# Kernel optimization log

Measured on AMD Instinct MI355X. Metric: run time of the kernel, lower is better.

Reference implementation:

```python
import jax, jax.numpy as jnp
import numpy as np

DIM = 2048
N_HEADS = 16
N_KV = 8
NUM_REP = N_HEADS // N_KV  # 2
HEAD_DIM = DIM // N_HEADS // 2  # 64
EPS = 1e-5
THETA = 10000.0
B, S = 2, 2048


def setup_inputs() -> dict:
    key = jax.random.key(0)
    ks = jax.random.split(key, 12)
    x = jax.random.normal(ks[0], (B, S, DIM), dtype=jnp.float32)
    wq = jax.random.normal(ks[1], (DIM, DIM), dtype=jnp.float32) * 0.02
    wk = jax.random.normal(ks[2], (DIM, DIM // NUM_REP), dtype=jnp.float32) * 0.02
    wv = jax.random.normal(ks[3], (DIM, DIM // NUM_REP), dtype=jnp.float32) * 0.02
    wo = jax.random.normal(ks[4], (DIM, DIM), dtype=jnp.float32) * 0.02
    lambda_q1 = jax.random.normal(ks[5], (HEAD_DIM,), dtype=jnp.float32) * 0.1
    lambda_k1 = jax.random.normal(ks[6], (HEAD_DIM,), dtype=jnp.float32) * 0.1
    lambda_q2 = jax.random.normal(ks[7], (HEAD_DIM,), dtype=jnp.float32) * 0.1
    lambda_k2 = jax.random.normal(ks[8], (HEAD_DIM,), dtype=jnp.float32) * 0.1
    lambda_init = jnp.array([0.8], dtype=jnp.float32)
    subln_w = jnp.ones((2 * HEAD_DIM,), dtype=jnp.float32)
    # rope tables: precompute_freqs_cis(dim=2*HEAD_DIM) then sliced to first HEAD_DIM//2 freqs
    exps = jnp.arange(0, HEAD_DIM, 2, dtype=jnp.float32) / (2.0 * HEAD_DIM)
    freqs = THETA ** (-exps)  # [HEAD_DIM//2]
    ang = jnp.arange(S, dtype=jnp.float32)[:, None] * freqs[None, :]  # [S, HEAD_DIM//2]
    return {
        "x": x, "wq": wq, "wk": wk, "wv": wv, "wo": wo,
        "lambda_q1": lambda_q1, "lambda_k1": lambda_k1,
        "lambda_q2": lambda_q2, "lambda_k2": lambda_k2,
        "lambda_init": lambda_init, "subln_w": subln_w,
        "freqs_cos": jnp.cos(ang), "freqs_sin": jnp.sin(ang),
    }


def _rope(t, cos, sin):
    # t: [B,S,H,hd]; cos/sin: [S, hd//2]; complex-pair rotation on (even, odd)
    e, o = t[..., 0::2], t[..., 1::2]
    c = cos[None, :, None, :]
    s = sin[None, :, None, :]
    return jnp.stack([e * c - o * s, e * s + o * c], axis=-1).reshape(t.shape)


def _repeat_kv_buggy(t, n_rep):
    # faithful to source: t is [B, n_kv, S, hd]; unsqueeze at dim 3 then reshape,
    # which flattens (n_kv, S, rep) -> (n_kv*rep, S)
    b, n_kv, slen, hd = t.shape
    exp = jnp.broadcast_to(t[:, :, :, None, :], (b, n_kv, slen, n_rep, hd))
    return exp.reshape(b, n_kv * n_rep, slen, hd)


def _attn(q, k, v, scale):
    # q,k: [B,H,S,hd]; v: [B,H,S,2hd]
    scores = jnp.einsum('bhqd,bhkd->bhqk', q, k) * scale
    p = jax.nn.softmax(scores, axis=-1)
    return jnp.einsum('bhqk,bhkd->bhqd', p, v)


def reference(x, wq, wk, wv, wo, lambda_q1, lambda_k1, lambda_q2, lambda_k2,
              lambda_init, subln_w, freqs_cos, freqs_sin):
    bsz, seqlen, _ = x.shape
    scale = HEAD_DIM ** -0.5
    q = (x @ wq).reshape(bsz, seqlen, 2 * N_HEADS, HEAD_DIM)
    k = (x @ wk).reshape(bsz, seqlen, 2 * N_KV, HEAD_DIM)
    v = (x @ wv).reshape(bsz, seqlen, N_KV, 2 * HEAD_DIM)
    q = _rope(q, freqs_cos, freqs_sin)
    k = _rope(k, freqs_cos, freqs_sin)
    q = q.reshape(bsz, seqlen, N_HEADS, 2, HEAD_DIM)
    k = k.reshape(bsz, seqlen, N_KV, 2, HEAD_DIM)
    q1 = q[:, :, :, 0].transpose(0, 2, 1, 3)  # [B,H,S,hd]
    q2 = q[:, :, :, 1].transpose(0, 2, 1, 3)
    k1 = _repeat_kv_buggy(k[:, :, :, 0].transpose(0, 2, 1, 3), NUM_REP)
    k2 = _repeat_kv_buggy(k[:, :, :, 1].transpose(0, 2, 1, 3), NUM_REP)
    vr = _repeat_kv_buggy(v.transpose(0, 2, 1, 3), NUM_REP)  # [B,H,S,2hd]
    attn1 = _attn(q1, k1, vr, scale)
    attn2 = _attn(q2, k2, vr, scale)
    lambda_1 = jnp.exp(jnp.sum(lambda_q1 * lambda_k1))
    lambda_2 = jnp.exp(jnp.sum(lambda_q2 * lambda_k2))
    lambda_full = lambda_1 - lambda_2 + lambda_init[0]
    attn = attn1 - lambda_full * attn2  # [B,H,S,2hd]
    # sub-layer RMSNorm over 2*HEAD_DIM
    rms = jax.lax.rsqrt(jnp.mean(attn * attn, axis=-1, keepdims=True) + EPS)
    attn = attn * rms * subln_w
    attn = attn * (1.0 - lambda_init[0])
    attn = attn.transpose(0, 2, 1, 3).reshape(bsz, seqlen, N_HEADS * 2 * HEAD_DIM)
    return attn @ wo
```

## Files before the change

kernel.cpp:

```cpp
#include <hip/hip_runtime.h>
#include <stdint.h>

typedef unsigned short u16;
typedef __attribute__((ext_vector_type(8))) short bf16x8v;
typedef __attribute__((ext_vector_type(4))) float f32x4;

#define DIM   2048
#define NH    16
#define NKV   8
#define HD    64
#define B_    2
#define S_    2048
#define ROWS  (B_*S_)
#define NQKV  4096
#define EPS_   1e-5f
#define SCALE_ 0.125f

__device__ __forceinline__ u16 bfbits(float f) {
  union { float f; unsigned int u; } a; a.f = f;
  unsigned int u = a.u;
  return (u16)((u + 0x7FFFu + ((u >> 16) & 1u)) >> 16);
}

__device__ __forceinline__ f32x4 mfma16(bf16x8v a, bf16x8v b, f32x4 c) {
  return __builtin_amdgcn_mfma_f32_16x16x32_bf16(a, b, c, 0, 0, 0);
}

__device__ __forceinline__ void gload_lds16(const void* g, void* l) {
  __builtin_amdgcn_global_load_lds(
      (const __attribute__((address_space(1))) unsigned int*)g,
      (__attribute__((address_space(3))) unsigned int*)l, 16, 0, 0);
}

__global__ void cast_f32_bf16(const float* __restrict__ src, u16* __restrict__ dst, int n4) {
  int i = blockIdx.x * 256 + threadIdx.x;
  if (i >= n4) return;
  float4 v = ((const float4*)src)[i];
  ushort4 o; o.x = bfbits(v.x); o.y = bfbits(v.y); o.z = bfbits(v.z); o.w = bfbits(v.w);
  ((ushort4*)dst)[i] = o;
}

__global__ void transpose_cast(const float* __restrict__ src, u16* __restrict__ dst, int R, int C) {
  __shared__ float t[32][33];
  int c0 = blockIdx.x * 32, r0 = blockIdx.y * 32;
  int x = threadIdx.x, y = threadIdx.y;
#pragma unroll
  for (int i = 0; i < 4; ++i) t[y + 8*i][x] = src[(size_t)(r0 + y + 8*i) * C + c0 + x];
  __syncthreads();
#pragma unroll
  for (int i = 0; i < 4; ++i) dst[(size_t)(c0 + y + 8*i) * R + r0 + x] = bfbits(t[x][y + 8*i]);
}

__global__ void v_transpose(const float* __restrict__ qkv, u16* __restrict__ Vt) {
  __shared__ float t[32][33];
  int z = blockIdx.z;
  int b = z >> 3, kv = z & 7;
  int s0 = blockIdx.x * 32, d0 = blockIdx.y * 32;
  int x = threadIdx.x, y = threadIdx.y;
  const float* src = qkv + (size_t)b * S_ * NQKV + 3072 + kv * 128;
#pragma unroll
  for (int i = 0; i < 4; ++i) t[y + 8*i][x] = src[(size_t)(s0 + y + 8*i) * NQKV + d0 + x];
  __syncthreads();
  u16* dst = Vt + ((size_t)(b * NKV + kv) * 128) * S_;
#pragma unroll
  for (int i = 0; i < 4; ++i) dst[(size_t)(d0 + y + 8*i) * S_ + s0 + x] = bfbits(t[x][y + 8*i]);
}

__global__ void rope_kernel(const float* __restrict__ qkv, const float* __restrict__ fc,
                            const float* __restrict__ fs, u16* __restrict__ D1, u16* __restrict__ D2,
                            int hshift, int coloff) {
  int p = blockIdx.x * 256 + threadIdx.x;
  int i = p & 31;
  int hh = (p >> 5) & ((1 << hshift) - 1);
  int row = p >> (5 + hshift);
  int s = row & (S_ - 1);
  int b = row >> 11;
  const float* src = qkv + (size_t)row * NQKV + coloff + hh * HD + 2 * i;
  float e = src[0], o = src[1];
  float c = fc[s * 32 + i], sn = fs[s * 32 + i];
  float r0 = e * c - o * sn, r1 = e * sn + o * c;
  u16* dst = (hh & 1) ? D2 : D1;
  int nh = 1 << (hshift - 1);
  size_t offo = (((size_t)b * nh + (hh >> 1)) * S_ + s) * HD + 2 * i;
  unsigned int packed = (unsigned int)bfbits(r0) | ((unsigned int)bfbits(r1) << 16);
  *(unsigned int*)(dst + offo) = packed;
}

__global__ void lambda_kernel(const float* lq1, const float* lk1, const float* lq2,
                              const float* lk2, const float* li, float* scal) {
  int t = threadIdx.x;
  float p1 = lq1[t] * lk1[t];
  float p2 = lq2[t] * lk2[t];
#pragma unroll
  for (int off = 32; off > 0; off >>= 1) { p1 += __shfl_xor(p1, off); p2 += __shfl_xor(p2, off); }
  if (t == 0) {
    scal[0] = __expf(p1) - __expf(p2) + li[0];
    scal[1] = 1.0f - li[0];
  }
}

template<int NI>
__global__ __launch_bounds__(512, 2) void gemm8p(const u16* __restrict__ A, const u16* __restrict__ Bt,
                                                 float* __restrict__ C, int M, int N, int K) {
  constexpr int BN = NI * 64;
  constexpr int BROUNDS = BN / 64;
  __shared__ u16 Al[2][256 * 64];
  __shared__ u16 Bl[2][BN * 64];
  const int tid = threadIdx.x;
  const int wid = tid >> 6, lane = tid & 63;
  const int wm = wid >> 2, wn = wid & 3;
  const int lr = lane & 15, cq = lane >> 4;
  const size_t row0 = (size_t)blockIdx.y * 256, col0 = (size_t)blockIdx.x * BN;

  f32x4 acc[8][NI];
#pragma unroll
  for (int i = 0; i < 8; ++i)
#pragma unroll
    for (int j = 0; j < NI; ++j) acc[i][j] = f32x4{0.f, 0.f, 0.f, 0.f};

  bf16x8v a[4][2], b0[NI / 2][2], b1[NI / 2][2];

  auto stageA = [&](int buf, int kt) {
#pragma unroll
    for (int rd = 0; rd < 4; ++rd) {
      int n = rd * 512 + tid;
      int r = n >> 3, c = (n & 7) ^ (r & 7);
      gload_lds16(A + (row0 + r) * (size_t)K + kt + c * 8,
                  (char*)&Al[buf][0] + (rd * 512 + wid * 64) * 16);
    }
  };
  auto stageB = [&](int buf, int kt) {
#pragma unroll
    for (int rd = 0; rd < BROUNDS; ++rd) {
      int n = rd * 512 + tid;
      int r = n >> 3, c = (n & 7) ^ (r & 7);
      gload_lds16(Bt + (col0 + r) * (size_t)K + kt + c * 8,
                  (char*)&Bl[buf][0] + (rd * 512 + wid * 64) * 16);
    }
  };
  auto readA = [&](int buf, int mh) {
#pragma unroll
    for (int m2 = 0; m2 < 4; ++m2)
#pragma unroll
      for (int ks = 0; ks < 2; ++ks) {
        int rt = wm * 128 + (mh * 4 + m2) * 16 + lr;
        a[m2][ks] = *(const bf16x8v*)&Al[buf][rt * 64 + (((ks * 4 + cq) ^ (rt & 7)) * 8)];
      }
  };
  auto readB = [&](int buf, int nh, bf16x8v (&bb)[NI / 2][2]) {
#pragma unroll
    for (int n2 = 0; n2 < NI / 2; ++n2)
#pragma unroll
      for (int ks = 0; ks < 2; ++ks) {
        int rt = wn * (NI * 16) + (nh * (NI / 2) + n2) * 16 + lr;
        bb[n2][ks] = *(const bf16x8v*)&Bl[buf][rt * 64 + (((ks * 4 + cq) ^ (rt & 7)) * 8)];
      }
  };
  auto mfmaq = [&](int mh, int nh, bf16x8v (&bb)[NI / 2][2]) {
    __builtin_amdgcn_s_barrier();
    asm volatile("s_waitcnt lgkmcnt(0)" ::: "memory");
    __builtin_amdgcn_sched_barrier(0);
    __builtin_amdgcn_s_setprio(1);
#pragma unroll
    for (int m2 = 0; m2 < 4; ++m2)
#pragma unroll
      for (int n2 = 0; n2 < NI / 2; ++n2)
#pragma unroll
        for (int ks = 0; ks < 2; ++ks)
          acc[mh * 4 + m2][nh * (NI / 2) + n2] =
              mfma16(a[m2][ks], bb[n2][ks], acc[mh * 4 + m2][nh * (NI / 2) + n2]);
    __builtin_amdgcn_s_setprio(0);
    __builtin_amdgcn_s_barrier();
  };
  auto vmwait = [&](bool last) {
    if (last) { asm volatile("s_waitcnt vmcnt(0)" ::: "memory"); }
    else {
      if constexpr (NI == 4) { asm volatile("s_waitcnt vmcnt(4)" ::: "memory"); }
      else                   { asm volatile("s_waitcnt vmcnt(2)" ::: "memory"); }
    }
  };

  stageA(0, 0);
  stageB(0, 0);
  stageB(1, 64);
  vmwait(false);
  __builtin_amdgcn_s_barrier();

  const int NITER = K >> 7;
  for (int it = 0; it < NITER; ++it) {
    const int kt = it << 7;
    const bool nl = (it < NITER - 1);
    readA(0, 0); readB(0, 0, b0);
    mfmaq(0, 0, b0);
    readB(0, 1, b1);
    stageA(1, kt + 64);
    mfmaq(0, 1, b1);
    readA(0, 1);
    if (nl) stageB(0, kt + 128);
    mfmaq(1, 1, b1);
    vmwait(!nl);
    mfmaq(1, 0, b0);
    readA(1, 0); readB(1, 0, b0);
    mfmaq(0, 0, b0);
    readB(1, 1, b1);
    if (nl) stageA(0, kt + 128);
    mfmaq(0, 1, b1);
    readA(1, 1);
    if (nl) stageB(1, kt + 192);
    mfmaq(1, 1, b1);
    vmwait(!nl);
    mfmaq(1, 0, b0);
  }

  const int crow = cq * 4;
#pragma unroll
  for (int mi = 0; mi < 8; ++mi)
#pragma unroll
    for (int ni = 0; ni < NI; ++ni) {
      float* cp = C + (row0 + wm * 128 + mi * 16 + crow) * (size_t)N + col0 + wn * (NI * 16) + ni * 16 + lr;
#pragma unroll
      for (int j = 0; j < 4; ++j) cp[(size_t)j * N] = acc[mi][ni][j];
    }
}

__device__ __forceinline__ void attn_step2(const u16* K1, const u16* K2, const u16* Vts,
                                           u16* Pw1, u16* Pw2,
                                           const bf16x8v* q1f, const bf16x8v* q2f,
                                           float* m1, float* l1, f32x4* O1,
                                           float* m2, float* l2, f32x4* O2,
                                           int lane) {
  const int lr = lane & 15, cq = lane >> 4, crow = cq * 4;
  f32x4 s1[4] = {}, s2[4] = {};
  __builtin_amdgcn_s_setprio(1);
#pragma unroll
  for (int kf = 0; kf < 4; ++kf) {
    const int row = kf * 16 + lr, sw = row & 7;
    const bf16x8v ka0 = *(const bf16x8v*)(K1 + row * 64 + ((cq ^ sw) * 8));
    const bf16x8v ka1 = *(const bf16x8v*)(K1 + row * 64 + (((cq + 4) ^ sw) * 8));
    const bf16x8v kb0 = *(const bf16x8v*)(K2 + row * 64 + ((cq ^ sw) * 8));
    const bf16x8v kb1 = *(const bf16x8v*)(K2 + row * 64 + (((cq + 4) ^ sw) * 8));
    s1[kf] = mfma16(q1f[0], ka0, s1[kf]);
    s2[kf] = mfma16(q2f[0], kb0, s2[kf]);
    s1[kf] = mfma16(q1f[1], ka1, s1[kf]);
    s2[kf] = mfma16(q2f[1], kb1, s2[kf]);
  }
  __builtin_amdgcn_s_setprio(0);
  float pm1[4], pm2[4];
#pragma unroll
  for (int j = 0; j < 4; ++j) { pm1[j] = -1e30f; pm2[j] = -1e30f; }
#pragma unroll
  for (int kf = 0; kf < 4; ++kf)
#pragma unroll
    for (int j = 0; j < 4; ++j) {
      float a = s1[kf][j] * SCALE_, b = s2[kf][j] * SCALE_;
      s1[kf][j] = a; s2[kf][j] = b;
      pm1[j] = fmaxf(pm1[j], a); pm2[j] = fmaxf(pm2[j], b);
    }
#pragma unroll
  for (int off = 1; off < 16; off <<= 1)
#pragma unroll
    for (int j = 0; j < 4; ++j) {
      pm1[j] = fmaxf(pm1[j], __shfl_xor(pm1[j], off));
      pm2[j] = fmaxf(pm2[j], __shfl_xor(pm2[j], off));
    }
  float al1[4], al2[4], ps1[4], ps2[4];
#pragma unroll
  for (int j = 0; j < 4; ++j) {
    float mn1 = fmaxf(m1[j], pm1[j]), mn2 = fmaxf(m2[j], pm2[j]);
    al1[j] = __expf(m1[j] - mn1);     al2[j] = __expf(m2[j] - mn2);
    m1[j] = mn1;                      m2[j] = mn2;
    ps1[j] = 0.f;                     ps2[j] = 0.f;
  }
#pragma unroll
  for (int kf = 0; kf < 4; ++kf)
#pragma unroll
    for (int j = 0; j < 4; ++j) {
      float p1 = __expf(s1[kf][j] - m1[j]);
      float p2 = __expf(s2[kf][j] - m2[j]);
      s1[kf][j] = p1; s2[kf][j] = p2;
      ps1[j] += p1;   ps2[j] += p2;
    }
#pragma unroll
  for (int off = 1; off < 16; off <<= 1)
#pragma unroll
    for (int j = 0; j < 4; ++j) {
      ps1[j] += __shfl_xor(ps1[j], off);
      ps2[j] += __shfl_xor(ps2[j], off);
    }
#pragma unroll
  for (int j = 0; j < 4; ++j) {
    l1[j] = l1[j] * al1[j] + ps1[j];
    l2[j] = l2[j] * al2[j] + ps2[j];
  }
#pragma unroll
  for (int f = 0; f < 8; ++f)
#pragma unroll
    for (int j = 0; j < 4; ++j) { O1[f][j] *= al1[j]; O2[f][j] *= al2[j]; }
#pragma unroll
  for (int kf = 0; kf < 4; ++kf) {
    const int ch = kf * 2 + (lr >> 3), cl = lr & 7;
#pragma unroll
    for (int j = 0; j < 4; ++j) {
      const int row = crow + j;
      const int o = row * 64 + ((ch ^ (row & 7)) * 8) + cl;
      Pw1[o] = bfbits(s1[kf][j]);
      Pw2[o] = bfbits(s2[kf][j]);
    }
  }
  __builtin_amdgcn_s_setprio(1);
#pragma unroll
  for (int kst = 0; kst < 2; ++kst) {
    const int po = lr * 64 + (((kst * 4 + cq) ^ (lr & 7)) * 8);
    bf16x8v pf1 = *(const bf16x8v*)(Pw1 + po);
    bf16x8v pf2 = *(const bf16x8v*)(Pw2 + po);
#pragma unroll
    for (int f = 0; f < 8; ++f) {
      const int row = f * 16 + lr;
      bf16x8v vf = *(const bf16x8v*)(Vts + row * 64 + (((kst * 4 + cq) ^ (row & 7)) * 8));
      O1[f] = mfma16(pf1, vf, O1[f]);
      O2[f] = mfma16(pf2, vf, O2[f]);
    }
  }
  __builtin_amdgcn_s_setprio(0);
}

__device__ __forceinline__ void stage_tile(const u16* k1b, const u16* k2b, const u16* vb,
                                           int key0, u16* K1d, u16* K2d, u16* Vd,
                                           int tid, int wave) {
#pragma unroll
  for (int i = 0; i < 2; ++i) {
    int n = i * 256 + tid;
    int r = n >> 3, cl = (n & 7) ^ (r & 7);
    gload_lds16(k1b + (size_t)(key0 + r) * HD + cl * 8, (char*)K1d + (i * 256 + wave * 64) * 16);
    gload_lds16(k2b + (size_t)(key0 + r) * HD + cl * 8, (char*)K2d + (i * 256 + wave * 64) * 16);
  }
#pragma unroll
  for (int i = 0; i < 4; ++i) {
    int n = i * 256 + tid;
    int r = n >> 3, cl = (n & 7) ^ (r & 7);
    gload_lds16(vb + (size_t)r * S_ + key0 + cl * 8, (char*)Vd + (i * 256 + wave * 64) * 16);
  }
}

__global__ __launch_bounds__(256) void attn_kernel(
    const u16* __restrict__ Q1, const u16* __restrict__ Q2,
    const u16* __restrict__ K1g, const u16* __restrict__ K2g,
    const u16* __restrict__ Vt, const float* __restrict__ scal,
    const float* __restrict__ subw, u16* __restrict__ attnb) {
  __shared__ u16 K1s[2][64 * 64];
  __shared__ u16 K2s[2][64 * 64];
  __shared__ u16 Vts[2][128 * 64];
  __shared__ u16 Ps1[4][16 * 64];
  __shared__ u16 Ps2[4][16 * 64];
  const int qb = blockIdx.x, h = blockIdx.y, b = blockIdx.z;
  const int tid = threadIdx.x;
  const int wave = tid >> 6, lane = tid & 63;
  const int lr = lane & 15, lkq = (lane >> 4) * 8;
  const int crow = (lane >> 4) * 4;
  const int kv = h >> 1;
  const int keybase = (h & 1) * 1024;

  const int srow = qb * 64 + wave * 16 + lr;
  const u16* q1p = Q1 + (((size_t)b * NH + h) * S_ + srow) * HD + lkq;
  const u16* q2p = Q2 + (((size_t)b * NH + h) * S_ + srow) * HD + lkq;
  bf16x8v q1f[2], q2f[2];
  q1f[0] = *(const bf16x8v*)(q1p);       q1f[1] = *(const bf16x8v*)(q1p + 32);
  q2f[0] = *(const bf16x8v*)(q2p);       q2f[1] = *(const bf16x8v*)(q2p + 32);

  f32x4 O1[8] = {}, O2[8] = {};
  float m1[4], l1[4], m2[4], l2[4];
#pragma unroll
  for (int j = 0; j < 4; ++j) { m1[j] = -1e30f; l1[j] = 0.f; m2[j] = -1e30f; l2[j] = 0.f; }

  const u16* k1b = K1g + ((size_t)b * NKV + kv) * S_ * HD;
  const u16* k2b = K2g + ((size_t)b * NKV + kv) * S_ * HD;
  const u16* vb  = Vt  + ((size_t)b * NKV + kv) * 128 * S_;

  stage_tile(k1b, k2b, vb, keybase, K1s[0], K2s[0], Vts[0], tid, wave);
  for (int ck = 0; ck < 16; ++ck) {
    const int cur = ck & 1;
    __syncthreads();
    if (ck < 15)
      stage_tile(k1b, k2b, vb, keybase + (ck + 1) * 64,
                 K1s[cur ^ 1], K2s[cur ^ 1], Vts[cur ^ 1], tid, wave);
    attn_step2(K1s[cur], K2s[cur], Vts[cur], Ps1[wave], Ps2[wave],
               q1f, q2f, m1, l1, O1, m2, l2, O2, lane);
  }

  const float lam = scal[0], ofac = scal[1];
  float ssq[4] = {0.f, 0.f, 0.f, 0.f};
#pragma unroll
  for (int f = 0; f < 8; ++f)
#pragma unroll
    for (int j = 0; j < 4; ++j) {
      float cv = O1[f][j] / l1[j] - lam * (O2[f][j] / l2[j]);
      O1[f][j] = cv;
      ssq[j] += cv * cv;
    }
#pragma unroll
  for (int off = 1; off < 16; off <<= 1)
#pragma unroll
    for (int j = 0; j < 4; ++j) ssq[j] += __shfl_xor(ssq[j], off);
  float rs[4];
#pragma unroll
  for (int j = 0; j < 4; ++j) rs[j] = rsqrtf(ssq[j] * (1.f / 128.f) + EPS_) * ofac;
  const size_t rowb = (size_t)b * S_ + qb * 64 + wave * 16 + crow;
#pragma unroll
  for (int f = 0; f < 8; ++f) {
    float sw = subw[f * 16 + lr];
#pragma unroll
    for (int j = 0; j < 4; ++j)
      attnb[(rowb + j) * DIM + h * 128 + f * 16 + lr] = bfbits(O1[f][j] * rs[j] * sw);
  }
}

extern "C" void kernel_launch(void* const* d_in, const int* in_sizes, int n_in,
                              void* d_out, int out_size, void* d_ws, size_t ws_size,
                              hipStream_t stream) {
  const float* x   = (const float*)d_in[0];
  const float* wq  = (const float*)d_in[1];
  const float* wk  = (const float*)d_in[2];
  const float* wv  = (const float*)d_in[3];
  const float* wo  = (const float*)d_in[4];
  const float* lq1 = (const float*)d_in[5];
  const float* lk1 = (const float*)d_in[6];
  const float* lq2 = (const float*)d_in[7];
  const float* lk2 = (const float*)d_in[8];
  const float* li  = (const float*)d_in[9];
  const float* subw= (const float*)d_in[10];
  const float* fc  = (const float*)d_in[11];
  const float* fs  = (const float*)d_in[12];
  float* out = (float*)d_out;

  char* ws = (char*)d_ws;
  size_t off = 0;
  auto alloc = [&](size_t bytes) { char* p = ws + off; off += (bytes + 255) & ~(size_t)255; return p; };
  u16*   xb    = (u16*)alloc((size_t)ROWS * DIM * 2);
  u16*   wqkvT = (u16*)alloc((size_t)NQKV * DIM * 2);
  u16*   woT   = (u16*)alloc((size_t)DIM * DIM * 2);
  float* qkv   = (float*)alloc((size_t)ROWS * NQKV * 4);
  u16*   Q1    = (u16*)alloc((size_t)B_ * NH * S_ * HD * 2);
  u16*   Q2    = (u16*)alloc((size_t)B_ * NH * S_ * HD * 2);
  u16*   K1    = (u16*)alloc((size_t)B_ * NKV * S_ * HD * 2);
  u16*   K2    = (u16*)alloc((size_t)B_ * NKV * S_ * HD * 2);
  u16*   Vt    = (u16*)alloc((size_t)B_ * NKV * 128 * S_ * 2);
  u16*   attnb = (u16*)alloc((size_t)ROWS * DIM * 2);
  float* scal  = (float*)alloc(256);

  cast_f32_bf16<<<ROWS * DIM / 4 / 256, 256, 0, stream>>>(x, xb, ROWS * DIM / 4);
  transpose_cast<<<dim3(64, 64), dim3(32, 8), 0, stream>>>(wq, wqkvT, DIM, DIM);
  transpose_cast<<<dim3(32, 64), dim3(32, 8), 0, stream>>>(wk, wqkvT + (size_t)2048 * DIM, DIM, 1024);
  transpose_cast<<<dim3(32, 64), dim3(32, 8), 0, stream>>>(wv, wqkvT + (size_t)3072 * DIM, DIM, 1024);
  transpose_cast<<<dim3(64, 64), dim3(32, 8), 0, stream>>>(wo, woT, DIM, DIM);

  gemm8p<4><<<dim3(NQKV / 256, ROWS / 256), 512, 0, stream>>>(xb, wqkvT, qkv, ROWS, NQKV, DIM);

  rope_kernel<<<ROWS * 32 * 32 / 256, 256, 0, stream>>>(qkv, fc, fs, Q1, Q2, 5, 0);
  rope_kernel<<<ROWS * 16 * 32 / 256, 256, 0, stream>>>(qkv, fc, fs, K1, K2, 4, 2048);
  v_transpose<<<dim3(64, 4, 16), dim3(32, 8), 0, stream>>>(qkv, Vt);
  lambda_kernel<<<1, 64, 0, stream>>>(lq1, lk1, lq2, lk2, li, scal);

  attn_kernel<<<dim3(32, NH, B_), 256, 0, stream>>>(Q1, Q2, K1, K2, Vt, scal, subw, attnb);

  gemm8p<2><<<dim3(DIM / 128, ROWS / 256), 512, 0, stream>>>(attnb, woT, out, ROWS, DIM, DIM);
}
```

Baseline: 495.1 us.

## Read K/V fragments directly from global memory in attention, drop LDS staging

Removes the double-buffered LDS staging of K1, K2 and V tiles and the per-chunk block barrier; each wave now loads its MFMA operands for K and transposed V straight from global memory. Launch bounds request three blocks per SM to raise occupancy now that shared memory use is small. The trade is that the four waves in a block no longer share staged tiles, so each reloads the same K/V data through the cache. The V loads are also strided by the sequence length, so loads become less coalesced and latency is exposed with no explicit prefetch.

New measurement: 798.0 us. 1.61x slower.

```diff
diff --git a/kernel.cpp b/kernel.cpp
--- a/kernel.cpp
+++ b/kernel.cpp
@@ -223,22 +223,23 @@
     }
 }
 
-__device__ __forceinline__ void attn_step2(const u16* K1, const u16* K2, const u16* Vts,
-                                           u16* Pw1, u16* Pw2,
-                                           const bf16x8v* q1f, const bf16x8v* q2f,
-                                           float* m1, float* l1, f32x4* O1,
-                                           float* m2, float* l2, f32x4* O2,
-                                           int lane) {
+__device__ __forceinline__ void attn_step2g(const u16* k1t, const u16* k2t, const u16* vt,
+                                            u16* Pw1, u16* Pw2,
+                                            const bf16x8v* q1f, const bf16x8v* q2f,
+                                            float* m1, float* l1, f32x4* O1,
+                                            float* m2, float* l2, f32x4* O2,
+                                            int lane) {
   const int lr = lane & 15, cq = lane >> 4, crow = cq * 4;
   f32x4 s1[4] = {}, s2[4] = {};
   __builtin_amdgcn_s_setprio(1);
 #pragma unroll
   for (int kf = 0; kf < 4; ++kf) {
-    const int row = kf * 16 + lr, sw = row & 7;
-    const bf16x8v ka0 = *(const bf16x8v*)(K1 + row * 64 + ((cq ^ sw) * 8));
-    const bf16x8v ka1 = *(const bf16x8v*)(K1 + row * 64 + (((cq + 4) ^ sw) * 8));
-    const bf16x8v kb0 = *(const bf16x8v*)(K2 + row * 64 + ((cq ^ sw) * 8));
-    const bf16x8v kb1 = *(const bf16x8v*)(K2 + row * 64 + (((cq + 4) ^ sw) * 8));
+    const u16* p1 = k1t + (kf * 16 + lr) * HD + cq * 8;
+    const u16* p2 = k2t + (kf * 16 + lr) * HD + cq * 8;
+    const bf16x8v ka0 = *(const bf16x8v*)(p1);
+    const bf16x8v ka1 = *(const bf16x8v*)(p1 + 32);
+    const bf16x8v kb0 = *(const bf16x8v*)(p2);
+    const bf16x8v kb1 = *(const bf16x8v*)(p2 + 32);
     s1[kf] = mfma16(q1f[0], ka0, s1[kf]);
     s2[kf] = mfma16(q2f[0], kb0, s2[kf]);
     s1[kf] = mfma16(q1f[1], ka1, s1[kf]);
@@ -315,8 +316,7 @@
     bf16x8v pf2 = *(const bf16x8v*)(Pw2 + po);
 #pragma unroll
     for (int f = 0; f < 8; ++f) {
-      const int row = f * 16 + lr;
-      bf16x8v vf = *(const bf16x8v*)(Vts + row * 64 + (((kst * 4 + cq) ^ (row & 7)) * 8));
+      bf16x8v vf = *(const bf16x8v*)(vt + (size_t)(f * 16 + lr) * S_ + kst * 32 + cq * 8);
       O1[f] = mfma16(pf1, vf, O1[f]);
       O2[f] = mfma16(pf2, vf, O2[f]);
     }
@@ -324,32 +324,11 @@
   __builtin_amdgcn_s_setprio(0);
 }
 
-__device__ __forceinline__ void stage_tile(const u16* k1b, const u16* k2b, const u16* vb,
-                                           int key0, u16* K1d, u16* K2d, u16* Vd,
-                                           int tid, int wave) {
-#pragma unroll
-  for (int i = 0; i < 2; ++i) {
-    int n = i * 256 + tid;
-    int r = n >> 3, cl = (n & 7) ^ (r & 7);
-    gload_lds16(k1b + (size_t)(key0 + r) * HD + cl * 8, (char*)K1d + (i * 256 + wave * 64) * 16);
-    gload_lds16(k2b + (size_t)(key0 + r) * HD + cl * 8, (char*)K2d + (i * 256 + wave * 64) * 16);
-  }
-#pragma unroll
-  for (int i = 0; i < 4; ++i) {
-    int n = i * 256 + tid;
-    int r = n >> 3, cl = (n & 7) ^ (r & 7);
-    gload_lds16(vb + (size_t)r * S_ + key0 + cl * 8, (char*)Vd + (i * 256 + wave * 64) * 16);
-  }
-}
-
-__global__ __launch_bounds__(256) void attn_kernel(
+__global__ __launch_bounds__(256, 3) void attn_kernel(
     const u16* __restrict__ Q1, const u16* __restrict__ Q2,
     const u16* __restrict__ K1g, const u16* __restrict__ K2g,
     const u16* __restrict__ Vt, const float* __restrict__ scal,
     const float* __restrict__ subw, u16* __restrict__ attnb) {
-  __shared__ u16 K1s[2][64 * 64];
-  __shared__ u16 K2s[2][64 * 64];
-  __shared__ u16 Vts[2][128 * 64];
   __shared__ u16 Ps1[4][16 * 64];
   __shared__ u16 Ps2[4][16 * 64];
   const int qb = blockIdx.x, h = blockIdx.y, b = blockIdx.z;
@@ -376,15 +355,10 @@
   const u16* k2b = K2g + ((size_t)b * NKV + kv) * S_ * HD;
   const u16* vb  = Vt  + ((size_t)b * NKV + kv) * 128 * S_;
 
-  stage_tile(k1b, k2b, vb, keybase, K1s[0], K2s[0], Vts[0], tid, wave);
   for (int ck = 0; ck < 16; ++ck) {
-    const int cur = ck & 1;
-    __syncthreads();
-    if (ck < 15)
-      stage_tile(k1b, k2b, vb, keybase + (ck + 1) * 64,
-                 K1s[cur ^ 1], K2s[cur ^ 1], Vts[cur ^ 1], tid, wave);
-    attn_step2(K1s[cur], K2s[cur], Vts[cur], Ps1[wave], Ps2[wave],
-               q1f, q2f, m1, l1, O1, m2, l2, O2, lane);
+    const int key0 = keybase + ck * 64;
+    attn_step2g(k1b + (size_t)key0 * HD, k2b + (size_t)key0 * HD, vb + key0,
+                Ps1[wave], Ps2[wave], q1f, q2f, m1, l1, O1, m2, l2, O2, lane);
   }
 
   const float lam = scal[0], ofac = scal[1];
```
